# Kernel optimization log

Measured on AMD Instinct MI355X. Metric: run time of the kernel, lower is better.

Reference implementation:

```python
import jax, jax.numpy as jnp
import numpy as np

NORM_EPS = 1e-6
QK_SCALE = 1.0 / 128.0  # 1/d_head (muP)
ROTARY_BASE = 10000
INFTY_APPROX = 1e30

B, T, M, H, D = 2, 2048, 1024, 8, 128


def _rmsnorm(x, eps=NORM_EPS):
    # normalize over the last (head) dim; no learned gains (norm_gains=False)
    ms = jnp.mean(jnp.square(x), axis=-1, keepdims=True)
    return x / jnp.sqrt(ms + eps)


def _rope(x, base=ROTARY_BASE):
    # x: [b, h, t, d]; rotate (even-half, odd-half) pairs as in the source
    length, width = x.shape[-2], x.shape[-1]
    half = width // 2
    pos = jnp.arange(length, dtype=x.dtype)[:, None]            # [t, 1]
    freqs = jnp.power(jnp.asarray(base, x.dtype), -jnp.arange(half, dtype=x.dtype) / half)[None, :]
    rad = pos * freqs                                            # [t, half]
    cos = jnp.cos(rad)[None, None]
    sin = jnp.sin(rad)[None, None]
    even, odd = jnp.split(x, 2, axis=-1)
    return jnp.concatenate([even * cos - odd * sin, even * sin + odd * cos], axis=-1)


def setup_inputs() -> dict:
    key = jax.random.key(0)
    ks = jax.random.split(key, 5)
    std = M ** -0.5
    return {
        "x": jax.random.normal(ks[0], (B, T, M), jnp.float32),
        "wq": jax.random.normal(ks[1], (M, H, D), jnp.float32) * std,
        "wk": jax.random.normal(ks[2], (M, H, D), jnp.float32) * std,
        "wv": jax.random.normal(ks[3], (M, H, D), jnp.float32) * std,
        "wo": jax.random.normal(ks[4], (H, D, M), jnp.float32) * std,
    }


def reference(x, wq, wk, wv, wo):
    # projections: [b, h, t, d]
    q = jnp.einsum('bim,mhd->bhid', x, wq)
    k = jnp.einsum('bim,mhd->bhid', x, wk)
    v = jnp.einsum('bim,mhd->bhid', x, wv)
    # qk RMSNorm (norm_gains=False)
    q = _rmsnorm(q)
    k = _rmsnorm(k)
    # inline RoPE
    q = _rope(q)
    k = _rope(k)
    # scaled scores: mult applied to both q and k (mult^2 = qk_scale)
    mult = jnp.asarray(QK_SCALE ** 0.5, q.dtype)
    s = jnp.einsum('bhid,bhjd->bhij', q * mult, k * mult)
    # causal mask: subtract large constant where i < j
    t = s.shape[-1]
    mask = (jnp.arange(t)[:, None] < jnp.arange(t)[None, :]).astype(s.dtype)
    s = s - jnp.asarray(INFTY_APPROX, s.dtype) * mask[None, None]
    p = jax.nn.softmax(s, axis=-1)
    o = jnp.einsum('bhij,bhjd->bhid', p, v)
    return jnp.einsum('bhid,hdm->bim', o, wo)
```

## Files before the change

kernel.cpp:

```cpp
#include <hip/hip_runtime.h>
#include <hip/hip_bf16.h>
#include <math.h>

#define B_  2
#define T_  2048
#define M_  1024
#define H_  8
#define D_  128
#define NROW (B_ * T_)
#define HD  (H_ * D_)

#define NORM_EPS 1e-6f
#define QK_MULT  0.08838834764831845f
#define LN_BASE_64 0.14391156510f

typedef short bf16x8  __attribute__((ext_vector_type(8)));
typedef float f32x4   __attribute__((ext_vector_type(4)));
typedef float f32x16  __attribute__((ext_vector_type(16)));
typedef unsigned int uint32x2 __attribute__((ext_vector_type(2)));

static __device__ __forceinline__ unsigned short f2bf(float f) {
    union { __hip_bfloat16 h; unsigned short u; } cv;
    cv.h = __float2bfloat16(f);
    return cv.u;
}
static __device__ __forceinline__ unsigned int pk2bf(float a, float b) {
    return ((unsigned int)f2bf(b) << 16) | f2bf(a);
}

static __device__ __forceinline__ void gload_lds16(const unsigned short* g,
                                                   unsigned short* l) {
    __builtin_amdgcn_global_load_lds(
        (const __attribute__((address_space(1))) void*)g,
        (__attribute__((address_space(3))) void*)l, 16, 0, 0);
}

__global__ __launch_bounds__(256) void prep(const float* __restrict__ x,
                                            const float* __restrict__ w0,
                                            const float* __restrict__ w1,
                                            const float* __restrict__ w2,
                                            const float* __restrict__ w3,
                                            unsigned short* __restrict__ xb,
                                            unsigned short* __restrict__ wqkvT,
                                            unsigned short* __restrict__ woT,
                                            int* __restrict__ ctr)
{
    __shared__ float t[32][33];
    const int z = blockIdx.z;
    if (z == 4) {
        if (blockIdx.x == 0 && blockIdx.y == 0 && threadIdx.x < 8)
            ctr[threadIdx.x] = 0;
        const size_t base = ((size_t)blockIdx.y * 32 + blockIdx.x) * 4096;
        #pragma unroll
        for (int it = 0; it < 4; ++it) {
            const size_t i = base + it * 1024 + threadIdx.x * 4;
            const float4 v = *(const float4*)(x + i);
            ushort4 o;
            o.x = f2bf(v.x); o.y = f2bf(v.y); o.z = f2bf(v.z); o.w = f2bf(v.w);
            *(ushort4*)(xb + i) = o;
        }
        return;
    }
    const float* in = z == 0 ? w0 : (z == 1 ? w1 : (z == 2 ? w2 : w3));
    unsigned short* out = z < 3 ? (wqkvT + (size_t)z * 1024 * 1024) : woT;

    const int tx = threadIdx.x & 31;
    const int ty = threadIdx.x >> 5;
    const int n0 = blockIdx.x * 32;
    const int k0 = blockIdx.y * 32;
    #pragma unroll
    for (int r = 0; r < 4; ++r)
        t[ty + r * 8][tx] = in[(size_t)(k0 + ty + r * 8) * 1024 + n0 + tx];
    __syncthreads();
    #pragma unroll
    for (int r = 0; r < 4; ++r)
        out[(size_t)(n0 + ty + r * 8) * 1024 + k0 + tx] = f2bf(t[tx][ty + r * 8]);
}

__global__ __launch_bounds__(256) void gemm_qkv(const unsigned short* __restrict__ A,
                                                const unsigned short* __restrict__ Bt,
                                                unsigned short* __restrict__ oq,
                                                unsigned short* __restrict__ ok,
                                                unsigned short* __restrict__ vt)
{
    __shared__ __align__(16) unsigned short smem[17408];
    #define AsQ(buf) (smem + (buf) * 4096)
    #define BsQ(buf) (smem + 8192 + (buf) * 4096)

    const int tid  = threadIdx.x;
    const int lane = tid & 63;
    const int w    = tid >> 6;
    const int g    = lane >> 4;
    const int lc   = lane & 15;

    const int m0 = blockIdx.y * 128;
    const int n0 = blockIdx.x * 128;

    const unsigned short* aBase = A  + (size_t)m0 * 1024;
    const unsigned short* bBase = Bt + (size_t)n0 * 1024;

    int dstOff[2];
    size_t srcOff[2];
    #pragma unroll
    for (int it = 0; it < 2; ++it) {
        const int u  = tid + it * 256;
        const int r2 = u >> 2;
        const int sg = (u & 3) ^ (r2 & 3);
        dstOff[it] = u * 8;
        srcOff[it] = (size_t)r2 * 1024 + sg * 8;
    }

    f32x4 acc[2][8];
    #pragma unroll
    for (int i = 0; i < 2; ++i)
        #pragma unroll
        for (int j = 0; j < 8; ++j)
            acc[i][j] = (f32x4){0.f, 0.f, 0.f, 0.f};

    #pragma unroll
    for (int it = 0; it < 2; ++it) {
        gload_lds16(aBase + srcOff[it], AsQ(0) + dstOff[it]);
        gload_lds16(bBase + srcOff[it], BsQ(0) + dstOff[it]);
    }

    for (int kt = 0; kt < 32; ++kt) {
        const int cur = kt & 1;
        __syncthreads();

        if (kt < 31) {
            const int k0n = (kt + 1) * 32;
            #pragma unroll
            for (int it = 0; it < 2; ++it) {
                gload_lds16(aBase + srcOff[it] + k0n, AsQ(cur ^ 1) + dstOff[it]);
                gload_lds16(bBase + srcOff[it] + k0n, BsQ(cur ^ 1) + dstOff[it]);
            }
        }

        const int sw = (g ^ (lc & 3)) << 3;
        bf16x8 af[2], bfr[8];
        #pragma unroll
        for (int i = 0; i < 2; ++i)
            af[i] = *(const bf16x8*)&AsQ(cur)[(w * 32 + i * 16 + lc) * 32 + sw];
        #pragma unroll
        for (int j = 0; j < 8; ++j)
            bfr[j] = *(const bf16x8*)&BsQ(cur)[(j * 16 + lc) * 32 + sw];

        #pragma unroll
        for (int i = 0; i < 2; ++i)
            #pragma unroll
            for (int j = 0; j < 8; ++j)
                acc[i][j] = __builtin_amdgcn_mfma_f32_16x16x32_bf16(af[i], bfr[j], acc[i][j], 0, 0, 0);
    }

    const int which = n0 >> 10;
    const int ncol0 = n0 & 1023;
    if (which < 2) {
        unsigned short* outp = which == 0 ? oq : ok;
        float freq[4];
        #pragma unroll
        for (int j = 0; j < 4; ++j)
            freq[j] = __expf(-(float)(j * 16 + lc) * LN_BASE_64);

        #pragma unroll
        for (int i = 0; i < 2; ++i)
            #pragma unroll
            for (int r = 0; r < 4; ++r) {
                float s = 0.f;
                #pragma unroll
                for (int j = 0; j < 8; ++j) s += acc[i][j][r] * acc[i][j][r];
                #pragma unroll
                for (int off = 1; off < 16; off <<= 1) s += __shfl_xor(s, off);
                const float rms = rsqrtf(s * (1.0f / 128.0f) + NORM_EPS) * QK_MULT;

                const int trow = m0 + w * 32 + i * 16 + g * 4 + r;
                const float tpos = (float)(trow & (T_ - 1));
                unsigned short* op = outp + (size_t)trow * 1024 + ncol0;
                #pragma unroll
                for (int j = 0; j < 4; ++j) {
                    float sn, cs;
                    __sincosf(tpos * freq[j], &sn, &cs);
                    const float e = acc[i][j][r] * rms;
                    const float o = acc[i][j + 4][r] * rms;
                    op[j * 16 + lc]      = f2bf(e * cs - o * sn);
                    op[j * 16 + lc + 64] = f2bf(e * sn + o * cs);
                }
            }
    } else {
        const int b2 = m0 >> 11;
        const int hh = ncol0 >> 7;
        const int PAD = 136;
        __syncthreads();
        #pragma unroll
        for (int i = 0; i < 2; ++i) {
            const int t0 = w * 32 + i * 16 + g * 4;
            #pragma unroll
            for (int j = 0; j < 8; ++j) {
                uint2 val;
                val.x = pk2bf(acc[i][j][0], acc[i][j][1]);
                val.y = pk2bf(acc[i][j][2], acc[i][j][3]);
                *(uint2*)&smem[(j * 16 + lc) * PAD + t0] = val;
            }
        }
        __syncthreads();
        const int row  = tid >> 1;
        const int half = tid & 1;
        const unsigned short* src = &smem[row * PAD + half * 64];
        unsigned short* dst = vt + ((size_t)(b2 * 8 + hh) * 128 + row) * T_
                                 + (m0 & 2047) + half * 64;
        #pragma unroll
        for (int it2 = 0; it2 < 8; ++it2)
            *(uint4*)(dst + it2 * 8) = *(const uint4*)(src + it2 * 8);
    }
    #undef AsQ
    #undef BsQ
}

__global__ __launch_bounds__(256) void gemm_out(const unsigned short* __restrict__ A,
                                                const unsigned short* __restrict__ Bt,
                                                float* __restrict__ cf)
{
    __shared__ unsigned short As[2][128 * 64];
    __shared__ unsigned short Bs[2][64 * 64];

    const int tid  = threadIdx.x;
    const int lane = tid & 63;
    const int w    = tid >> 6;
    const int g    = lane >> 4;
    const int lc   = lane & 15;
    const int wm   = w >> 1;
    const int wn   = w & 1;

    const int m0 = blockIdx.y * 128;
    const int n0 = blockIdx.x * 64;

    const unsigned short* aBase = A  + (size_t)m0 * 1024;
    const unsigned short* bBase = Bt + (size_t)n0 * 1024;

    int dstA[4], dstB[2];
    size_t srcA[4], srcB[2];
    #pragma unroll
    for (int it = 0; it < 4; ++it) {
        const int u  = tid + it * 256;
        const int r2 = u >> 3;
        const int sg = (u & 7) ^ (r2 & 7);
        dstA[it] = u * 8;
        srcA[it] = (size_t)r2 * 1024 + sg * 8;
    }
    #pragma unroll
    for (int it = 0; it < 2; ++it) {
        const int u  = tid + it * 256;
        const int r2 = u >> 3;
        const int sg = (u & 7) ^ (r2 & 7);
        dstB[it] = u * 8;
        srcB[it] = (size_t)r2 * 1024 + sg * 8;
    }

    f32x4 acc[4][2];
    #pragma unroll
    for (int i = 0; i < 4; ++i)
        #pragma unroll
        for (int j = 0; j < 2; ++j)
            acc[i][j] = (f32x4){0.f, 0.f, 0.f, 0.f};

    #pragma unroll
    for (int it = 0; it < 4; ++it)
        gload_lds16(aBase + srcA[it], &As[0][dstA[it]]);
    #pragma unroll
    for (int it = 0; it < 2; ++it)
        gload_lds16(bBase + srcB[it], &Bs[0][dstB[it]]);

    for (int kt = 0; kt < 16; ++kt) {
        const int cur = kt & 1;
        __syncthreads();

        if (kt < 15) {
            const int k0n = (kt + 1) * 64;
            #pragma unroll
            for (int it = 0; it < 4; ++it)
                gload_lds16(aBase + srcA[it] + k0n, &As[cur ^ 1][dstA[it]]);
            #pragma unroll
            for (int it = 0; it < 2; ++it)
                gload_lds16(bBase + srcB[it] + k0n, &Bs[cur ^ 1][dstB[it]]);
        }

        #pragma unroll
        for (int dc = 0; dc < 2; ++dc) {
            const int sw = ((dc * 4 + g) ^ (lc & 7)) << 3;
            bf16x8 af[4], bfr[2];
            #pragma unroll
            for (int i = 0; i < 4; ++i)
                af[i] = *(const bf16x8*)&As[cur][(wm * 64 + i * 16 + lc) * 64 + sw];
            #pragma unroll
            for (int j = 0; j < 2; ++j)
                bfr[j] = *(const bf16x8*)&Bs[cur][(wn * 32 + j * 16 + lc) * 64 + sw];

            #pragma unroll
            for (int i = 0; i < 4; ++i)
                #pragma unroll
                for (int j = 0; j < 2; ++j)
                    acc[i][j] = __builtin_amdgcn_mfma_f32_16x16x32_bf16(af[i], bfr[j], acc[i][j], 0, 0, 0);
        }
    }

    #pragma unroll
    for (int i = 0; i < 4; ++i) {
        const int mrow = m0 + wm * 64 + i * 16 + g * 4;
        #pragma unroll
        for (int j = 0; j < 2; ++j) {
            const int nc = n0 + wn * 32 + j * 16 + lc;
            #pragma unroll
            for (int r = 0; r < 4; ++r)
                cf[(size_t)(mrow + r) * 1024 + nc] = acc[i][j][r];
        }
    }
}

__global__ __launch_bounds__(256) void flash_attn(const unsigned short* __restrict__ qb,
                                                  const unsigned short* __restrict__ kb,
                                                  const unsigned short* __restrict__ vt,
                                                  unsigned short* __restrict__ o,
                                                  int* __restrict__ ctr)
{
    __shared__ __align__(16) unsigned short smem[2 * 64 * 128 + 2 * 128 * 64 + 128];
    __shared__ int unitLds;
    unsigned short* KsB = smem;
    unsigned short* VsB = smem + 2 * 64 * 128;
    float* lscr = (float*)(smem + 2 * 64 * 128 + 2 * 128 * 64);
    float* scr  = (float*)smem;

    const int tid  = threadIdx.x;
    const int lane = tid & 63;
    const int w    = tid >> 6;
    const int wj   = w >> 1;
    const int wq2  = w & 1;
    const int qcol = lane & 31;
    const int hi   = lane >> 5;

    const int p = blockIdx.x & 7;

    int mI[4];
    size_t srcKoff[4], srcVoff[4];
    #pragma unroll
    for (int it = 0; it < 4; ++it) {
        const int m = (w * 4 + it) * 64 + lane;
        mI[it] = m;
        const int jK = m >> 4, cK = (m & 15) ^ (jK & 15);
        srcKoff[it] = (size_t)jK * 1024 + cK * 8;
        const int dV = m >> 3, cV = (m & 7) ^ (dV & 7);
        srcVoff[it] = (size_t)dV * T_ + cV * 8;
    }

    for (;;) {
        if (tid == 0) unitLds = atomicAdd(&ctr[p], 1);
        __syncthreads();
        const int u = unitLds;
        if (u >= 64) break;
        const int qt = 31 - (u >> 1);
        const int bh = p + 8 * (u & 1);
        const int q0 = qt * 64;
        const int h  = bh & (H_ - 1);
        const int b  = bh >> 3;

        const size_t bhbase  = (size_t)b * T_ * HD + (size_t)h * 128;
        const size_t bhvbase = (size_t)bh * 128 * T_;
        const unsigned short* kgb = kb + bhbase;
        const unsigned short* vgb = vt + bhvbase;

        bf16x8 qf[8];
        {
            const unsigned short* qp = qb + bhbase + (size_t)(q0 + wq2 * 32 + qcol) * 1024 + hi * 8;
            #pragma unroll
            for (int ks = 0; ks < 8; ++ks)
                qf[ks] = *(const bf16x8*)(qp + ks * 16);
        }

        float lsum = 0.f;
        f32x16 otacc[4];
        #pragma unroll
        for (int dch = 0; dch < 4; ++dch)
            #pragma unroll
            for (int r = 0; r < 16; ++r) otacc[dch][r] = 0.f;

        #pragma unroll
        for (int it = 0; it < 4; ++it) {
            gload_lds16(kgb + srcKoff[it], &KsB[mI[it] * 8]);
            gload_lds16(vgb + srcVoff[it], &VsB[mI[it] * 8]);
        }

        for (int jt = 0; jt <= qt; ++jt) {
            const int cur = jt & 1;
            unsigned short* Ks = KsB + cur * (64 * 128);
            unsigned short* Vs = VsB + cur * (128 * 64);
            __syncthreads();

            if (jt < qt) {
                const size_t j0n = (size_t)(jt + 1) * 64;
                unsigned short* Kn = KsB + (cur ^ 1) * (64 * 128);
                unsigned short* Vn = VsB + (cur ^ 1) * (128 * 64);
                #pragma unroll
                for (int it = 0; it < 4; ++it) {
                    gload_lds16(kgb + j0n * 1024 + srcKoff[it], &Kn[mI[it] * 8]);
                    gload_lds16(vgb + j0n + srcVoff[it], &Vn[mI[it] * 8]);
                }
            }

            const bool dead = (jt == qt) && (wj > wq2);
            if (!dead) {
                const int jrow = wj * 32 + qcol;

                bf16x8 kf[8], vf[8];
                #pragma unroll
                for (int ks = 0; ks < 8; ++ks) {
                    const int c = ks * 2 + hi;
                    kf[ks] = *(const bf16x8*)&Ks[(jrow * 16 + (c ^ (lane & 15))) * 8];
                }
                #pragma unroll
                for (int ks2 = 0; ks2 < 2; ++ks2)
                    #pragma unroll
                    for (int dch = 0; dch < 4; ++dch) {
                        const int c = wj * 4 + ks2 * 2 + hi;
                        const int drow = dch * 32 + qcol;
                        vf[ks2 * 4 + dch] = *(const bf16x8*)&Vs[(drow * 8 + (c ^ (lane & 7))) * 8];
                    }

                f32x16 sacc0, sacc1;
                #pragma unroll
                for (int r = 0; r < 16; ++r) { sacc0[r] = 0.f; sacc1[r] = 0.f; }
                __builtin_amdgcn_s_setprio(1);
                #pragma unroll
                for (int ks = 0; ks < 8; ks += 2) {
                    sacc0 = __builtin_amdgcn_mfma_f32_32x32x16_bf16(kf[ks], qf[ks], sacc0, 0, 0, 0);
                    sacc1 = __builtin_amdgcn_mfma_f32_32x32x16_bf16(kf[ks + 1], qf[ks + 1], sacc1, 0, 0, 0);
                }
                __builtin_amdgcn_s_setprio(0);
                f32x16 sacc = sacc0 + sacc1;

                if (jt == qt && wj == wq2) {
                    #pragma unroll
                    for (int r = 0; r < 16; ++r) {
                        const int jl = (r & 3) + 8 * (r >> 2) + 4 * hi;
                        if (qcol < jl) sacc[r] = -1e30f;
                    }
                }

                unsigned int dw[8];
                #pragma unroll
                for (int m2 = 0; m2 < 8; ++m2) {
                    const float p0 = __expf(sacc[2 * m2]);
                    const float p1 = __expf(sacc[2 * m2 + 1]);
                    lsum += p0 + p1;
                    dw[m2] = pk2bf(p0, p1);
                }

                __builtin_amdgcn_s_setprio(1);
                #pragma unroll
                for (int ks2 = 0; ks2 < 2; ++ks2) {
                    const uint32x2 s02 = __builtin_amdgcn_permlane32_swap(
                        dw[4 * ks2 + 0], dw[4 * ks2 + 2], 0, 0);
                    const uint32x2 s13 = __builtin_amdgcn_permlane32_swap(
                        dw[4 * ks2 + 1], dw[4 * ks2 + 3], 0, 0);
                    union { unsigned int u2[4]; bf16x8 v; } pf;
                    pf.u2[0] = s02[0];
                    pf.u2[1] = s13[0];
                    pf.u2[2] = s02[1];
                    pf.u2[3] = s13[1];
                    #pragma unroll
                    for (int dch = 0; dch < 4; ++dch)
                        otacc[dch] = __builtin_amdgcn_mfma_f32_32x32x16_bf16(vf[ks2 * 4 + dch], pf.v, otacc[dch], 0, 0, 0);
                }
                __builtin_amdgcn_s_setprio(0);
            }
        }

        lsum += __shfl_xor(lsum, 32);
        __syncthreads();

        if (wj == 1) {
            float* s0 = scr + (size_t)(wq2 * 32 + qcol) * 129;
            #pragma unroll
            for (int dch = 0; dch < 4; ++dch)
                #pragma unroll
                for (int r = 0; r < 16; ++r)
                    s0[dch * 32 + (r & 3) + 8 * (r >> 2) + 4 * hi] = otacc[dch][r];
            if (hi == 0) lscr[wq2 * 32 + qcol] = lsum;
        }
        __syncthreads();
        if (wj == 0) {
            const float l = lsum + lscr[wq2 * 32 + qcol];
            const float inv = 1.0f / l;
            const float* s0 = scr + (size_t)(wq2 * 32 + qcol) * 129;
            unsigned short* op = o + bhbase + (size_t)(q0 + wq2 * 32 + qcol) * 1024;
            #pragma unroll
            for (int dch = 0; dch < 4; ++dch) {
                #pragma unroll
                for (int k4 = 0; k4 < 4; ++k4) {
                    const int d0 = dch * 32 + 8 * k4 + 4 * hi;
                    const float f0 = (otacc[dch][4 * k4 + 0] + s0[d0 + 0]) * inv;
                    const float f1 = (otacc[dch][4 * k4 + 1] + s0[d0 + 1]) * inv;
                    const float f2 = (otacc[dch][4 * k4 + 2] + s0[d0 + 2]) * inv;
                    const float f3 = (otacc[dch][4 * k4 + 3] + s0[d0 + 3]) * inv;
                    uint2 val;
                    val.x = pk2bf(f0, f1);
                    val.y = pk2bf(f2, f3);
                    *(uint2*)(op + d0) = val;
                }
            }
        }
        __syncthreads();
    }
}

extern "C" void kernel_launch(void* const* d_in, const int* in_sizes, int n_in,
                              void* d_out, int out_size, void* d_ws, size_t ws_size,
                              hipStream_t stream)
{
    const float* x  = (const float*)d_in[0];
    const float* wq = (const float*)d_in[1];
    const float* wk = (const float*)d_in[2];
    const float* wv = (const float*)d_in[3];
    const float* wo = (const float*)d_in[4];
    float* out = (float*)d_out;

    const size_t SZ = (size_t)NROW * HD;
    unsigned short* qb    = (unsigned short*)d_ws;
    unsigned short* kb    = qb + SZ;
    unsigned short* vt    = kb + SZ;
    unsigned short* ob    = vt + SZ;
    unsigned short* xb    = ob + SZ;
    unsigned short* wqkvT = xb + SZ;
    unsigned short* woT   = wqkvT + 3 * 1024 * 1024;
    int* ctr = (int*)out;

    prep<<<dim3(32, 32, 5), 256, 0, stream>>>(x, wq, wk, wv, wo, xb, wqkvT, woT, ctr);

    gemm_qkv<<<dim3(24, 32), 256, 0, stream>>>(xb, wqkvT, qb, kb, vt);

    flash_attn<<<dim3(512), 256, 0, stream>>>(qb, kb, vt, ob, ctr);

    gemm_out<<<dim3(16, 32), 256, 0, stream>>>(ob, woT, out);
}
```

Measured before the change: 193.1 us.

## Pair causal query tiles per block statically with four-stage K/V pipeline

Replaces the atomic work-counter scheduler in the attention kernel with a static assignment. Each of 256 blocks processes a short and a long query tile (qt and 31-qt) of one head, so every block does a balanced 33 K/V tiles in one continuous loop. The K/V staging moves from double to quad buffering with a vmcnt-based wait, which deepens prefetch, and the counter reset in prep is removed. The cost is more LDS per block, which may lower occupancy, plus an extra finalize step in the middle of the loop.

```diff
diff --git a/kernel.cpp b/kernel.cpp
--- a/kernel.cpp
+++ b/kernel.cpp
@@ -42,14 +42,11 @@
                                             const float* __restrict__ w3,
                                             unsigned short* __restrict__ xb,
                                             unsigned short* __restrict__ wqkvT,
-                                            unsigned short* __restrict__ woT,
-                                            int* __restrict__ ctr)
+                                            unsigned short* __restrict__ woT)
 {
     __shared__ float t[32][33];
     const int z = blockIdx.z;
     if (z == 4) {
-        if (blockIdx.x == 0 && blockIdx.y == 0 && threadIdx.x < 8)
-            ctr[threadIdx.x] = 0;
         const size_t base = ((size_t)blockIdx.y * 32 + blockIdx.x) * 4096;
         #pragma unroll
         for (int it = 0; it < 4; ++it) {
@@ -318,15 +315,10 @@
 __global__ __launch_bounds__(256) void flash_attn(const unsigned short* __restrict__ qb,
                                                   const unsigned short* __restrict__ kb,
                                                   const unsigned short* __restrict__ vt,
-                                                  unsigned short* __restrict__ o,
-                                                  int* __restrict__ ctr)
+                                                  unsigned short* __restrict__ o)
 {
-    __shared__ __align__(16) unsigned short smem[2 * 64 * 128 + 2 * 128 * 64 + 128];
-    __shared__ int unitLds;
-    unsigned short* KsB = smem;
-    unsigned short* VsB = smem + 2 * 64 * 128;
-    float* lscr = (float*)(smem + 2 * 64 * 128 + 2 * 128 * 64);
-    float* scr  = (float*)smem;
+    __shared__ __align__(16) unsigned short smem[4 * 16384 + 128];
+    float* lscr = (float*)(smem + 4 * 16384);
 
     const int tid  = threadIdx.x;
     const int lane = tid & 63;
@@ -336,7 +328,16 @@
     const int qcol = lane & 31;
     const int hi   = lane >> 5;
 
-    const int p = blockIdx.x & 7;
+    const int bid = blockIdx.x;
+    const int s   = bid >> 3;
+    const int bh  = (bid & 7) + 8 * (s & 1);
+    const int qtA = s >> 1;
+    const int qtB = 31 - qtA;
+    const int h   = bh & (H_ - 1);
+    const int b   = bh >> 3;
+
+    const size_t bhbase  = (size_t)b * T_ * HD + (size_t)h * 128;
+    const size_t bhvbase = (size_t)bh * 128 * T_;
 
     int mI[4];
     size_t srcKoff[4], srcVoff[4];
@@ -349,149 +350,191 @@
         const int dV = m >> 3, cV = (m & 7) ^ (dV & 7);
         srcVoff[it] = (size_t)dV * T_ + cV * 8;
     }
-
-    for (;;) {
-        if (tid == 0) unitLds = atomicAdd(&ctr[p], 1);
-        __syncthreads();
-        const int u = unitLds;
-        if (u >= 64) break;
-        const int qt = 31 - (u >> 1);
-        const int bh = p + 8 * (u & 1);
-        const int q0 = qt * 64;
-        const int h  = bh & (H_ - 1);
-        const int b  = bh >> 3;
-
-        const size_t bhbase  = (size_t)b * T_ * HD + (size_t)h * 128;
-        const size_t bhvbase = (size_t)bh * 128 * T_;
-        const unsigned short* kgb = kb + bhbase;
-        const unsigned short* vgb = vt + bhvbase;
-
-        bf16x8 qf[8];
+    const unsigned short* kgb = kb + bhbase;
+    const unsigned short* vgb = vt + bhvbase;
+
+#define SRCU(s_) ((s_) > qtA ? (s_) - qtA - 1 : (s_))
+#define STAGE(js_, bf_) {                                                    \
+        const size_t jo = (size_t)(js_) * 64;                                \
+        unsigned short* Kd = smem + (bf_) * 16384;                           \
+        unsigned short* Vd = Kd + 8192;                                      \
+        _Pragma("unroll")                                                    \
+        for (int it = 0; it < 4; ++it)                                       \
+            gload_lds16(kgb + jo * 1024 + srcKoff[it], &Kd[mI[it] * 8]);     \
+        _Pragma("unroll")                                                    \
+        for (int it = 0; it < 4; ++it)                                       \
+            gload_lds16(vgb + jo + srcVoff[it], &Vd[mI[it] * 8]);            \
+    }
+
+    bf16x8 qf[8];
+    {
+        const unsigned short* qp = qb + bhbase
+            + (size_t)(qtA * 64 + wq2 * 32 + qcol) * 1024 + hi * 8;
+        #pragma unroll
+        for (int ks = 0; ks < 8; ++ks)
+            qf[ks] = *(const bf16x8*)(qp + ks * 16);
+    }
+
+    float lsum = 0.f;
+    f32x16 otacc[4];
+    #pragma unroll
+    for (int dch = 0; dch < 4; ++dch)
+        #pragma unroll
+        for (int r = 0; r < 16; ++r) otacc[dch][r] = 0.f;
+
+    STAGE(SRCU(0), 0);
+    STAGE(SRCU(1), 1);
+    STAGE(SRCU(2), 2);
+
+    for (int u = 0; u < 33; ++u) {
+        asm volatile("s_waitcnt vmcnt(16)" ::: "memory");
+        __builtin_amdgcn_s_barrier();
         {
-            const unsigned short* qp = qb + bhbase + (size_t)(q0 + wq2 * 32 + qcol) * 1024 + hi * 8;
+            const int sn = u + 3 <= 32 ? u + 3 : 32;
+            STAGE(SRCU(sn), (u + 3) & 3);
+        }
+
+        unsigned short* Ks = smem + (u & 3) * 16384;
+        unsigned short* Vs = Ks + 8192;
+
+        const bool atD  = (u == qtA) || (u == 32);
+        const bool dead = atD && (wj > wq2);
+        if (!dead) {
+            const int jrow = wj * 32 + qcol;
+
+            bf16x8 kf[8], vf[8];
+            #pragma unroll
+            for (int ks = 0; ks < 8; ++ks) {
+                const int c = ks * 2 + hi;
+                kf[ks] = *(const bf16x8*)&Ks[(jrow * 16 + (c ^ (lane & 15))) * 8];
+            }
+            #pragma unroll
+            for (int ks2 = 0; ks2 < 2; ++ks2)
+                #pragma unroll
+                for (int dch = 0; dch < 4; ++dch) {
+                    const int c = wj * 4 + ks2 * 2 + hi;
+                    const int drow = dch * 32 + qcol;
+                    vf[ks2 * 4 + dch] = *(const bf16x8*)&Vs[(drow * 8 + (c ^ (lane & 7))) * 8];
+                }
+
+            f32x16 sacc0, sacc1;
+            #pragma unroll
+            for (int r = 0; r < 16; ++r) { sacc0[r] = 0.f; sacc1[r] = 0.f; }
+            __builtin_amdgcn_s_setprio(1);
+            #pragma unroll
+            for (int ks = 0; ks < 8; ks += 2) {
+                sacc0 = __builtin_amdgcn_mfma_f32_32x32x16_bf16(kf[ks], qf[ks], sacc0, 0, 0, 0);
+                sacc1 = __builtin_amdgcn_mfma_f32_32x32x16_bf16(kf[ks + 1], qf[ks + 1], sacc1, 0, 0, 0);
+            }
+            __builtin_amdgcn_s_setprio(0);
+            f32x16 sacc = sacc0 + sacc1;
+
+            if (atD && wj == wq2) {
+                #pragma unroll
+                for (int r = 0; r < 16; ++r) {
+                    const int jl = (r & 3) + 8 * (r >> 2) + 4 * hi;
+                    if (qcol < jl) sacc[r] = -1e30f;
+                }
+            }
+
+            unsigned int dw[8];
+            #pragma unroll
+            for (int m2 = 0; m2 < 8; ++m2) {
+                const float p0 = __expf(sacc[2 * m2]);
+                const float p1 = __expf(sacc[2 * m2 + 1]);
+                lsum += p0 + p1;
+                dw[m2] = pk2bf(p0, p1);
+            }
+
+            __builtin_amdgcn_s_setprio(1);
+            #pragma unroll
+            for (int ks2 = 0; ks2 < 2; ++ks2) {
+                const uint32x2 s02 = __builtin_amdgcn_permlane32_swap(
+                    dw[4 * ks2 + 0], dw[4 * ks2 + 2], 0, 0);
+                const uint32x2 s13 = __builtin_amdgcn_permlane32_swap(
+                    dw[4 * ks2 + 1], dw[4 * ks2 + 3], 0, 0);
+                union { unsigned int u2[4]; bf16x8 v; } pf;
+                pf.u2[0] = s02[0];
+                pf.u2[1] = s13[0];
+                pf.u2[2] = s02[1];
+                pf.u2[3] = s13[1];
+                #pragma unroll
+                for (int dch = 0; dch < 4; ++dch)
+                    otacc[dch] = __builtin_amdgcn_mfma_f32_32x32x16_bf16(vf[ks2 * 4 + dch], pf.v, otacc[dch], 0, 0, 0);
+            }
+            __builtin_amdgcn_s_setprio(0);
+        }
+
+        if (u == qtA) {
+            float* scr = (float*)(smem + (u & 3) * 16384);
+            lsum += __shfl_xor(lsum, 32);
+            __syncthreads();
+            const int row = wq2 * 32 + qcol;
+            if (wj == 1) {
+                float* s0 = scr + (size_t)row * 128;
+                #pragma unroll
+                for (int dch = 0; dch < 4; ++dch)
+                    #pragma unroll
+                    for (int r = 0; r < 16; ++r)
+                        s0[dch * 32 + (r & 3) + 8 * (r >> 2) + 4 * hi] = otacc[dch][r];
+                if (hi == 0) lscr[row] = lsum;
+            }
+            __syncthreads();
+            if (wj == 0) {
+                const float l = lsum + lscr[row];
+                const float inv = 1.0f / l;
+                const float* s0 = scr + (size_t)row * 128;
+                unsigned short* op = o + bhbase + (size_t)(qtA * 64 + row) * 1024;
+                #pragma unroll
+                for (int dch = 0; dch < 4; ++dch)
+                    #pragma unroll
+                    for (int k4 = 0; k4 < 4; ++k4) {
+                        const int d0 = dch * 32 + 8 * k4 + 4 * hi;
+                        const float f0 = (otacc[dch][4 * k4 + 0] + s0[d0 + 0]) * inv;
+                        const float f1 = (otacc[dch][4 * k4 + 1] + s0[d0 + 1]) * inv;
+                        const float f2 = (otacc[dch][4 * k4 + 2] + s0[d0 + 2]) * inv;
+                        const float f3 = (otacc[dch][4 * k4 + 3] + s0[d0 + 3]) * inv;
+                        uint2 val;
+                        val.x = pk2bf(f0, f1);
+                        val.y = pk2bf(f2, f3);
+                        *(uint2*)(op + d0) = val;
+                    }
+            }
+            lsum = 0.f;
+            #pragma unroll
+            for (int dch = 0; dch < 4; ++dch)
+                #pragma unroll
+                for (int r = 0; r < 16; ++r) otacc[dch][r] = 0.f;
+            const unsigned short* qp = qb + bhbase
+                + (size_t)(qtB * 64 + wq2 * 32 + qcol) * 1024 + hi * 8;
             #pragma unroll
             for (int ks = 0; ks < 8; ++ks)
                 qf[ks] = *(const bf16x8*)(qp + ks * 16);
         }
-
-        float lsum = 0.f;
-        f32x16 otacc[4];
-        #pragma unroll
-        for (int dch = 0; dch < 4; ++dch)
-            #pragma unroll
-            for (int r = 0; r < 16; ++r) otacc[dch][r] = 0.f;
-
-        #pragma unroll
-        for (int it = 0; it < 4; ++it) {
-            gload_lds16(kgb + srcKoff[it], &KsB[mI[it] * 8]);
-            gload_lds16(vgb + srcVoff[it], &VsB[mI[it] * 8]);
-        }
-
-        for (int jt = 0; jt <= qt; ++jt) {
-            const int cur = jt & 1;
-            unsigned short* Ks = KsB + cur * (64 * 128);
-            unsigned short* Vs = VsB + cur * (128 * 64);
-            __syncthreads();
-
-            if (jt < qt) {
-                const size_t j0n = (size_t)(jt + 1) * 64;
-                unsigned short* Kn = KsB + (cur ^ 1) * (64 * 128);
-                unsigned short* Vn = VsB + (cur ^ 1) * (128 * 64);
-                #pragma unroll
-                for (int it = 0; it < 4; ++it) {
-                    gload_lds16(kgb + j0n * 1024 + srcKoff[it], &Kn[mI[it] * 8]);
-                    gload_lds16(vgb + j0n + srcVoff[it], &Vn[mI[it] * 8]);
-                }
-            }
-
-            const bool dead = (jt == qt) && (wj > wq2);
-            if (!dead) {
-                const int jrow = wj * 32 + qcol;
-
-                bf16x8 kf[8], vf[8];
-                #pragma unroll
-                for (int ks = 0; ks < 8; ++ks) {
-                    const int c = ks * 2 + hi;
-                    kf[ks] = *(const bf16x8*)&Ks[(jrow * 16 + (c ^ (lane & 15))) * 8];
-                }
-                #pragma unroll
-                for (int ks2 = 0; ks2 < 2; ++ks2)
-                    #pragma unroll
-                    for (int dch = 0; dch < 4; ++dch) {
-                        const int c = wj * 4 + ks2 * 2 + hi;
-                        const int drow = dch * 32 + qcol;
-                        vf[ks2 * 4 + dch] = *(const bf16x8*)&Vs[(drow * 8 + (c ^ (lane & 7))) * 8];
-                    }
-
-                f32x16 sacc0, sacc1;
-                #pragma unroll
-                for (int r = 0; r < 16; ++r) { sacc0[r] = 0.f; sacc1[r] = 0.f; }
-                __builtin_amdgcn_s_setprio(1);
-                #pragma unroll
-                for (int ks = 0; ks < 8; ks += 2) {
-                    sacc0 = __builtin_amdgcn_mfma_f32_32x32x16_bf16(kf[ks], qf[ks], sacc0, 0, 0, 0);
-                    sacc1 = __builtin_amdgcn_mfma_f32_32x32x16_bf16(kf[ks + 1], qf[ks + 1], sacc1, 0, 0, 0);
-                }
-                __builtin_amdgcn_s_setprio(0);
-                f32x16 sacc = sacc0 + sacc1;
-
-                if (jt == qt && wj == wq2) {
-                    #pragma unroll
-                    for (int r = 0; r < 16; ++r) {
-                        const int jl = (r & 3) + 8 * (r >> 2) + 4 * hi;
-                        if (qcol < jl) sacc[r] = -1e30f;
-                    }
-                }
-
-                unsigned int dw[8];
-                #pragma unroll
-                for (int m2 = 0; m2 < 8; ++m2) {
-                    const float p0 = __expf(sacc[2 * m2]);
-                    const float p1 = __expf(sacc[2 * m2 + 1]);
-                    lsum += p0 + p1;
-                    dw[m2] = pk2bf(p0, p1);
-                }
-
-                __builtin_amdgcn_s_setprio(1);
-                #pragma unroll
-                for (int ks2 = 0; ks2 < 2; ++ks2) {
-                    const uint32x2 s02 = __builtin_amdgcn_permlane32_swap(
-                        dw[4 * ks2 + 0], dw[4 * ks2 + 2], 0, 0);
-                    const uint32x2 s13 = __builtin_amdgcn_permlane32_swap(
-                        dw[4 * ks2 + 1], dw[4 * ks2 + 3], 0, 0);
-                    union { unsigned int u2[4]; bf16x8 v; } pf;
-                    pf.u2[0] = s02[0];
-                    pf.u2[1] = s13[0];
-                    pf.u2[2] = s02[1];
-                    pf.u2[3] = s13[1];
-                    #pragma unroll
-                    for (int dch = 0; dch < 4; ++dch)
-                        otacc[dch] = __builtin_amdgcn_mfma_f32_32x32x16_bf16(vf[ks2 * 4 + dch], pf.v, otacc[dch], 0, 0, 0);
-                }
-                __builtin_amdgcn_s_setprio(0);
-            }
-        }
-
+    }
+
+    {
+        float* scr = (float*)smem;
         lsum += __shfl_xor(lsum, 32);
         __syncthreads();
-
+        const int row = wq2 * 32 + qcol;
         if (wj == 1) {
-            float* s0 = scr + (size_t)(wq2 * 32 + qcol) * 129;
+            float* s0 = scr + (size_t)row * 128;
             #pragma unroll
             for (int dch = 0; dch < 4; ++dch)
                 #pragma unroll
                 for (int r = 0; r < 16; ++r)
                     s0[dch * 32 + (r & 3) + 8 * (r >> 2) + 4 * hi] = otacc[dch][r];
-            if (hi == 0) lscr[wq2 * 32 + qcol] = lsum;
+            if (hi == 0) lscr[row] = lsum;
         }
         __syncthreads();
         if (wj == 0) {
-            const float l = lsum + lscr[wq2 * 32 + qcol];
+            const float l = lsum + lscr[row];
             const float inv = 1.0f / l;
-            const float* s0 = scr + (size_t)(wq2 * 32 + qcol) * 129;
-            unsigned short* op = o + bhbase + (size_t)(q0 + wq2 * 32 + qcol) * 1024;
-            #pragma unroll
-            for (int dch = 0; dch < 4; ++dch) {
+            const float* s0 = scr + (size_t)row * 128;
+            unsigned short* op = o + bhbase + (size_t)(qtB * 64 + row) * 1024;
+            #pragma unroll
+            for (int dch = 0; dch < 4; ++dch)
                 #pragma unroll
                 for (int k4 = 0; k4 < 4; ++k4) {
                     const int d0 = dch * 32 + 8 * k4 + 4 * hi;
@@ -504,10 +547,10 @@
                     val.y = pk2bf(f2, f3);
                     *(uint2*)(op + d0) = val;
                 }
-            }
-        }
-        __syncthreads();
-    }
+        }
+    }
+#undef STAGE
+#undef SRCU
 }
 
 extern "C" void kernel_launch(void* const* d_in, const int* in_sizes, int n_in,
@@ -529,13 +572,12 @@
     unsigned short* xb    = ob + SZ;
     unsigned short* wqkvT = xb + SZ;
     unsigned short* woT   = wqkvT + 3 * 1024 * 1024;
-    int* ctr = (int*)out;
-
-    prep<<<dim3(32, 32, 5), 256, 0, stream>>>(x, wq, wk, wv, wo, xb, wqkvT, woT, ctr);
+
+    prep<<<dim3(32, 32, 5), 256, 0, stream>>>(x, wq, wk, wv, wo, xb, wqkvT, woT);
 
     gemm_qkv<<<dim3(24, 32), 256, 0, stream>>>(xb, wqkvT, qb, kb, vt);
 
-    flash_attn<<<dim3(512), 256, 0, stream>>>(qb, kb, vt, ob, ctr);
+    flash_attn<<<dim3(256), 256, 0, stream>>>(qb, kb, vt, ob);
 
     gemm_out<<<dim3(16, 32), 256, 0, stream>>>(ob, woT, out);
 }
```

Result: no change. 191.0 us (-1.1%).
